# Kernel optimization log

Hardware: AMD Instinct MI355X
Metric: run time of the kernel (lower is better)

Reference implementation:

```python
import jax, jax.numpy as jnp
import numpy as np

G = 4       # num_groups
EPS = 1e-5  # BatchNorm eps


def setup_inputs() -> dict:
    key = jax.random.key(0)
    ks = jax.random.split(key, 8)
    B, C, T, V, K = 64, 256, 128, 25, 3
    dk = C // (G * 4)  # reduce_ratio=4 -> dk=16, dk*G=64
    return {
        "x": jax.random.normal(ks[0], (B, C, T, V), dtype=jnp.float32),
        "A": jax.random.uniform(ks[1], (K, V, V), dtype=jnp.float32),
        "Wq": jax.random.normal(ks[2], (dk * G, C), dtype=jnp.float32) * 0.05,
        "Wk": jax.random.normal(ks[3], (dk * G, C), dtype=jnp.float32) * 0.05,
        "Wconv": jax.random.normal(ks[4], (K, G, C // G, C // G), dtype=jnp.float32) * 0.05,
        "alpha": jnp.full((1,), 0.1, dtype=jnp.float32),
        "gamma": jax.random.uniform(ks[5], (C,), dtype=jnp.float32) + 0.5,
        "beta": jax.random.normal(ks[6], (C,), dtype=jnp.float32) * 0.1,
        "running_mean": jnp.zeros((C,), dtype=jnp.float32),
        "running_var": jnp.ones((C,), dtype=jnp.float32),
    }


def reference(x, A, Wq, Wk, Wconv, alpha, gamma, beta, running_mean, running_var):
    B, C, T, V = x.shape
    K = A.shape[0]
    dk = Wq.shape[0] // G
    Cg = C // G

    # Row-normalized fixed adjacency subsets (done in torch __init__)
    A_norm = A / jnp.clip(A.sum(-1, keepdims=True), 1e-6)  # (K,V,V)

    # Q/K 1x1 convs, temporal mean, per-group attention over joints
    q = jnp.einsum('oc,bctv->bov', Wq, x) / T  # conv then mean over T
    k = jnp.einsum('oc,bctv->bov', Wk, x) / T
    q = q.reshape(B, G, dk, V)
    k = k.reshape(B, G, dk, V)
    A_dyn = jnp.einsum('bgdv,bgdw->bgvw', q, k) / jnp.sqrt(jnp.float32(dk))
    A_dyn = jax.nn.softmax(A_dyn, axis=-1).mean(axis=1)  # (B,V,V)

    al = jnp.tanh(alpha[0])
    out = jnp.zeros_like(x)
    for k_idx in range(K):
        A_k = A_norm[k_idx][None] + al * A_dyn               # (B,V,V)
        x_agg = jnp.einsum('bvw,bctw->bctv', A_k, x)         # spatial aggregation
        xg = x_agg.reshape(B, G, Cg, T, V)
        y = jnp.einsum('goc,bgctv->bgotv', Wconv[k_idx], xg).reshape(B, C, T, V)
        out = out + y

    # BatchNorm2d in eval mode (running stats)
    inv = gamma / jnp.sqrt(running_var + EPS)
    bn = out * inv[None, :, None, None] + (beta - running_mean * inv)[None, :, None, None]
    return x + bn
```

## Files before the change

kernel.cpp:

```cpp
#include <hip/hip_runtime.h>

typedef __bf16 bf16x8 __attribute__((ext_vector_type(8)));
typedef __bf16 bf16x4 __attribute__((ext_vector_type(4)));
typedef float  f32x4  __attribute__((ext_vector_type(4)));


__global__ __launch_bounds__(256)
void k_tmean4(const float* __restrict__ x, float* __restrict__ xm)
{
    const int bid = blockIdx.x;
    const int b = bid >> 7, c2 = bid & 127;
    const int tid = threadIdx.x;
    const int c_loc = tid >> 7, r = tid & 127;

    __shared__ float xpart[2][25][5][4];

    if (r < 125) {
        const float* base = x + (size_t)(b * 256 + c2 * 2 + c_loc) * 3200;
        f32x4 acc = {0.f, 0.f, 0.f, 0.f};
#pragma unroll
        for (int i = 0; i < 7; ++i) {
            const int q = r + 125 * i;
            if (q < 800) {
                f32x4 v4 = *(const f32x4*)(base + q * 4);
                acc += v4;
            }
        }
        const int vq = r % 25, jg = r / 25;
        *(f32x4*)(&xpart[c_loc][vq][jg][0]) = acc;
    }
    __syncthreads();
    if (tid < 50) {
        const int cl = tid / 25, v = tid - cl * 25;
        float s = 0.f;
#pragma unroll
        for (int e = 0; e < 4; ++e) {
            const int vq = (((v - e + 25) % 25) * 19) % 25;
#pragma unroll
            for (int j = 0; j < 5; ++j) s += xpart[cl][vq][j][e];
        }
        xm[((size_t)(b * 256) + c2 * 2 + cl) * 25 + v] = s * (1.0f / 128.0f);
    }
}

__global__ __launch_bounds__(256)
void k_adyn(const float* __restrict__ xm, const float* __restrict__ A,
            const float* __restrict__ Wq, const float* __restrict__ Wk,
            const float* __restrict__ alpha, __bf16* __restrict__ afull,
            const float* __restrict__ Wconv, __bf16* __restrict__ wcb)
{
    const int b = blockIdx.x, tid = threadIdx.x;
    __shared__ float xm_s[256 * 25];
    __shared__ float q_s[64 * 25];
    __shared__ float k_s[64 * 25];
    __shared__ float sm_s[4][25][25];
    __shared__ float ad_s[25][25];
    __shared__ float rs_s[3][25];

    for (int i = tid; i < 768; i += 256)
        wcb[b * 768 + i] = (__bf16)Wconv[b * 768 + i];

    for (int i = tid; i < 256 * 25; i += 256) xm_s[i] = xm[(size_t)b * 6400 + i];
    for (int i = tid; i < 75; i += 256) {
        int k3 = i / 25, v = i - (i / 25) * 25;
        float s = 0.f;
        for (int w = 0; w < 25; ++w) s += A[(k3 * 25 + v) * 25 + w];
        rs_s[k3][v] = fmaxf(s, 1e-6f);
    }
    __syncthreads();

    for (int i = tid; i < 1600; i += 256) {
        int o = i / 25, v = i - o * 25;
        const float* wq = Wq + o * 256;
        const float* wk = Wk + o * 256;
        float aq = 0.f, ak = 0.f;
        for (int c4 = 0; c4 < 256; c4 += 4) {
            f32x4 q4 = *(const f32x4*)(wq + c4);
            f32x4 k4 = *(const f32x4*)(wk + c4);
#pragma unroll
            for (int e = 0; e < 4; ++e) {
                const float xv = xm_s[(c4 + e) * 25 + v];
                aq += q4[e] * xv;
                ak += k4[e] * xv;
            }
        }
        q_s[i] = aq; k_s[i] = ak;
    }
    __syncthreads();

    if (tid < 100) {
        int g = tid / 25, v = tid - (tid / 25) * 25;
        float l[25];
#pragma unroll
        for (int w = 0; w < 25; ++w) {
            float s = 0.f;
#pragma unroll
            for (int d = 0; d < 16; ++d)
                s += q_s[(g * 16 + d) * 25 + v] * k_s[(g * 16 + d) * 25 + w];
            l[w] = s * 0.25f;
        }
        float mx = l[0];
#pragma unroll
        for (int w = 1; w < 25; ++w) mx = fmaxf(mx, l[w]);
        float den = 0.f;
#pragma unroll
        for (int w = 0; w < 25; ++w) { l[w] = expf(l[w] - mx); den += l[w]; }
        float rden = 1.f / den;
#pragma unroll
        for (int w = 0; w < 25; ++w) sm_s[g][v][w] = l[w] * rden;
    }
    __syncthreads();
    for (int i = tid; i < 625; i += 256) {
        int v = i / 25, w = i - (i / 25) * 25;
        ad_s[v][w] = 0.25f * (sm_s[0][v][w] + sm_s[1][v][w] + sm_s[2][v][w] + sm_s[3][v][w]);
    }
    __syncthreads();

    const float al = tanhf(alpha[0]);
    for (int i = tid; i < 3 * 32 * 32; i += 256) {
        int k3 = i >> 10, rem = i & 1023, v = rem >> 5, w = rem & 31;
        float val = 0.f;
        if (v < 25 && w < 25)
            val = A[(k3 * 25 + v) * 25 + w] / rs_s[k3][v] + al * ad_s[v][w];
        afull[(size_t)b * 3072 + i] = (__bf16)val;
    }
}

__global__ __launch_bounds__(256, 4)
void k_main7(const float* __restrict__ x, const __bf16* __restrict__ wcb,
             const __bf16* __restrict__ afull,
             const float* __restrict__ gamma, const float* __restrict__ beta,
             const float* __restrict__ rmean, const float* __restrict__ rvar,
             float* __restrict__ out)
{
    const int orig = ((blockIdx.x & 7) << 10) | (blockIdx.x >> 3);
    const int tt = orig & 31;
    const int g  = (orig >> 5) & 3;
    const int b  = orig >> 7;
    const int tid = threadIdx.x;
    const int wave = tid >> 6;
    const int lane = tid & 63;
    const int l15 = lane & 15;
    const int lg  = lane >> 4;

    __shared__ __bf16 xs[64 * 4 * 32];
    __shared__ __bf16 xagg[112 * 64];

    {
        const int c = tid >> 2, t = tid & 3;
        const float* p = x + ((size_t)(b * 256 + g * 64 + c) * 128 + tt * 4 + t) * 25;
        float r[25];
#pragma unroll
        for (int j = 0; j < 25; ++j) r[j] = p[j];
        const int rowg = (c * 4 + t) << 2;
        const int sw = c & 7;
#pragma unroll
        for (int ch = 0; ch < 4; ++ch) {
            bf16x8 h;
#pragma unroll
            for (int e = 0; e < 8; ++e) {
                const int v = ch * 8 + e;
                h[e] = (v < 25) ? (__bf16)r[v] : (__bf16)0.f;
            }
            *(bf16x8*)((char*)xs + (((rowg | ch) ^ sw) << 4)) = h;
        }
    }

    const int o_lane = (wave << 4) + l15;
    const int ch = g * 64 + o_lane;
    const float inv  = gamma[ch] / sqrtf(rvar[ch] + 1e-5f);
    const float bias = beta[ch] - rmean[ch] * inv;

    const __bf16* ab = afull + ((size_t)(b * 3) << 10) + l15 * 32 + lg * 8;
    const __bf16* wb = wcb + (size_t)(g * 64 + o_lane) * 64 + lg * 8;

    __syncthreads();

    bf16x8 xfrag[4];
#pragma unroll
    for (int m = 0; m < 4; ++m) {
        const int c = m * 16 + l15;
        xfrag[m] = *(const bf16x8*)((char*)xs +
                      (((((c * 4 + wave) << 2) | lg) ^ (c & 7)) << 4));
    }

    f32x4 acc[7];
#pragma unroll
    for (int i = 0; i < 7; ++i) acc[i] = (f32x4){0.f, 0.f, 0.f, 0.f};
    const f32x4 zero4 = {0.f, 0.f, 0.f, 0.f};

#pragma unroll
    for (int k3 = 0; k3 < 3; ++k3) {
        bf16x8 bA[2], wf[2];
        bA[0] = *(const bf16x8*)(ab + (size_t)k3 * 1024);
        bA[1] = *(const bf16x8*)(ab + (size_t)k3 * 1024 + 512);
        wf[0] = *(const bf16x8*)(wb + (size_t)k3 * 16384);
        wf[1] = *(const bf16x8*)(wb + (size_t)k3 * 16384 + 32);

        if (k3 > 0) __syncthreads();

#pragma unroll
        for (int m = 0; m < 4; ++m) {
#pragma unroll
            for (int n = 0; n < 2; ++n) {
                f32x4 d = __builtin_amdgcn_mfma_f32_16x16x32_bf16(xfrag[m], bA[n],
                                                                  zero4, 0, 0, 0);
                const int v = n * 16 + l15;
                if (v < 25) {
                    const int cc  = wave * 25 + v;
                    const int col = (m * 16 + lg * 4) ^ ((cc & 7) << 3);
                    bf16x4 h;
                    h[0] = (__bf16)d[0]; h[1] = (__bf16)d[1];
                    h[2] = (__bf16)d[2]; h[3] = (__bf16)d[3];
                    *(bf16x4*)((char*)xagg + cc * 128 + col * 2) = h;
                }
            }
        }
        __syncthreads();

#pragma unroll
        for (int mcc = 0; mcc < 7; ++mcc) {
            const int cc = mcc * 16 + l15;
            const int sw2 = (cc & 7) << 3;
#pragma unroll
            for (int ks = 0; ks < 2; ++ks) {
                const int col = (ks * 32 + lg * 8) ^ sw2;
                bf16x8 aF = *(const bf16x8*)((char*)xagg + cc * 128 + col * 2);
                acc[mcc] = __builtin_amdgcn_mfma_f32_16x16x32_bf16(aF, wf[ks],
                                                                   acc[mcc], 0, 0, 0);
            }
        }
        if (k3 < 2) __syncthreads();
    }

    const size_t obase = (size_t)(b * 256 + ch) * 3200 + tt * 100;
#pragma unroll
    for (int mcc = 0; mcc < 7; ++mcc) {
        const int cc0 = mcc * 16 + lg * 4;
        if (cc0 < 100) {
            f32x4 o4;
#pragma unroll
            for (int j = 0; j < 4; ++j) {
                const int cc = cc0 + j;
                const int t = cc / 25, v = cc - t * 25;
                const int gr = (((o_lane * 4 + t) << 2) | (v >> 3)) ^ (o_lane & 7);
                const float xr = (float)*(const __bf16*)((char*)xs + (gr << 4) + ((v & 7) << 1));
                o4[j] = xr + acc[mcc][j] * inv + bias;
            }
            *(f32x4*)(out + obase + cc0) = o4;
        }
    }
}

extern "C" void kernel_launch(void* const* d_in, const int* in_sizes, int n_in,
                              void* d_out, int out_size, void* d_ws, size_t ws_size,
                              hipStream_t stream) {
    const float* x     = (const float*)d_in[0];
    const float* A     = (const float*)d_in[1];
    const float* Wq    = (const float*)d_in[2];
    const float* Wk    = (const float*)d_in[3];
    const float* Wconv = (const float*)d_in[4];
    const float* alpha = (const float*)d_in[5];
    const float* gamma = (const float*)d_in[6];
    const float* beta  = (const float*)d_in[7];
    const float* rmean = (const float*)d_in[8];
    const float* rvar  = (const float*)d_in[9];
    float* out = (float*)d_out;

    float*  xm    = (float*)d_ws;
    __bf16* afull = (__bf16*)((char*)d_ws + 1638400);
    __bf16* wcb   = (__bf16*)((char*)d_ws + 2031616);

    k_tmean4<<<64 * 128, 256, 0, stream>>>(x, xm);
    k_adyn<<<64, 256, 0, stream>>>(xm, A, Wq, Wk, alpha, afull, Wconv, wcb);
    k_main7<<<64 * 4 * 32, 256, 0, stream>>>(x, wcb, afull, gamma, beta,
                                             rmean, rvar, out);
}
```

Measured before the change: 193.0 us.

## Process two time tiles per block with prefetch of the next x tile

Each block of the main kernel now handles two consecutive 4-step time tiles instead of one, halving the grid size. The global load of the second tile's x values into registers is issued during the first tile's compute and then written to shared memory after the first output store. The aim is to hide global load latency and amortize per-block setup (BN params, weight/adjacency fragments) across two tiles. The cost is more register pressure from the extra 25-float prefetch buffer, extra barriers, and fewer blocks to fill the GPU.

New measurement: 344.8 us. 1.79x slower.

```diff
diff --git a/kernel.cpp b/kernel.cpp
--- a/kernel.cpp
+++ b/kernel.cpp
@@ -127,16 +127,16 @@
 }
 
 __global__ __launch_bounds__(256, 4)
-void k_main7(const float* __restrict__ x, const __bf16* __restrict__ wcb,
-             const __bf16* __restrict__ afull,
-             const float* __restrict__ gamma, const float* __restrict__ beta,
-             const float* __restrict__ rmean, const float* __restrict__ rvar,
-             float* __restrict__ out)
+void k_main11(const float* __restrict__ x, const __bf16* __restrict__ wcb,
+              const __bf16* __restrict__ afull,
+              const float* __restrict__ gamma, const float* __restrict__ beta,
+              const float* __restrict__ rmean, const float* __restrict__ rvar,
+              float* __restrict__ out)
 {
-    const int orig = ((blockIdx.x & 7) << 10) | (blockIdx.x >> 3);
-    const int tt = orig & 31;
-    const int g  = (orig >> 5) & 3;
-    const int b  = orig >> 7;
+    const int orig = ((blockIdx.x & 7) << 9) | (blockIdx.x >> 3);
+    const int tt2 = orig & 15;
+    const int g   = (orig >> 4) & 3;
+    const int b   = orig >> 6;
     const int tid = threadIdx.x;
     const int wave = tid >> 6;
     const int lane = tid & 63;
@@ -146,14 +146,14 @@
     __shared__ __bf16 xs[64 * 4 * 32];
     __shared__ __bf16 xagg[112 * 64];
 
+    const int c_st = tid >> 2, t_st = tid & 3;
+    const float* pbase = x + ((size_t)(b * 256 + g * 64 + c_st) * 128 + tt2 * 8 + t_st) * 25;
+    const int rowg = (c_st * 4 + t_st) << 2;
+    const int sw = c_st & 7;
     {
-        const int c = tid >> 2, t = tid & 3;
-        const float* p = x + ((size_t)(b * 256 + g * 64 + c) * 128 + tt * 4 + t) * 25;
         float r[25];
 #pragma unroll
-        for (int j = 0; j < 25; ++j) r[j] = p[j];
-        const int rowg = (c * 4 + t) << 2;
-        const int sw = c & 7;
+        for (int j = 0; j < 25; ++j) r[j] = pbase[j];
 #pragma unroll
         for (int ch = 0; ch < 4; ++ch) {
             bf16x8 h;
@@ -167,87 +167,112 @@
     }
 
     const int o_lane = (wave << 4) + l15;
-    const int ch = g * 64 + o_lane;
-    const float inv  = gamma[ch] / sqrtf(rvar[ch] + 1e-5f);
-    const float bias = beta[ch] - rmean[ch] * inv;
+    const int ch_o = g * 64 + o_lane;
+    const float inv  = gamma[ch_o] / sqrtf(rvar[ch_o] + 1e-5f);
+    const float bias = beta[ch_o] - rmean[ch_o] * inv;
 
     const __bf16* ab = afull + ((size_t)(b * 3) << 10) + l15 * 32 + lg * 8;
     const __bf16* wb = wcb + (size_t)(g * 64 + o_lane) * 64 + lg * 8;
 
     __syncthreads();
 
-    bf16x8 xfrag[4];
-#pragma unroll
-    for (int m = 0; m < 4; ++m) {
-        const int c = m * 16 + l15;
-        xfrag[m] = *(const bf16x8*)((char*)xs +
-                      (((((c * 4 + wave) << 2) | lg) ^ (c & 7)) << 4));
-    }
-
-    f32x4 acc[7];
-#pragma unroll
-    for (int i = 0; i < 7; ++i) acc[i] = (f32x4){0.f, 0.f, 0.f, 0.f};
-    const f32x4 zero4 = {0.f, 0.f, 0.f, 0.f};
-
-#pragma unroll
-    for (int k3 = 0; k3 < 3; ++k3) {
-        bf16x8 bA[2], wf[2];
-        bA[0] = *(const bf16x8*)(ab + (size_t)k3 * 1024);
-        bA[1] = *(const bf16x8*)(ab + (size_t)k3 * 1024 + 512);
-        wf[0] = *(const bf16x8*)(wb + (size_t)k3 * 16384);
-        wf[1] = *(const bf16x8*)(wb + (size_t)k3 * 16384 + 32);
-
-        if (k3 > 0) __syncthreads();
-
+    float r2[25];
+
+#pragma unroll 1
+    for (int it = 0; it < 2; ++it) {
+        bf16x8 xfrag[4];
 #pragma unroll
         for (int m = 0; m < 4; ++m) {
-#pragma unroll
-            for (int n = 0; n < 2; ++n) {
-                f32x4 d = __builtin_amdgcn_mfma_f32_16x16x32_bf16(xfrag[m], bA[n],
-                                                                  zero4, 0, 0, 0);
-                const int v = n * 16 + l15;
-                if (v < 25) {
-                    const int cc  = wave * 25 + v;
-                    const int col = (m * 16 + lg * 4) ^ ((cc & 7) << 3);
-                    bf16x4 h;
-                    h[0] = (__bf16)d[0]; h[1] = (__bf16)d[1];
-                    h[2] = (__bf16)d[2]; h[3] = (__bf16)d[3];
-                    *(bf16x4*)((char*)xagg + cc * 128 + col * 2) = h;
+            const int c = m * 16 + l15;
+            xfrag[m] = *(const bf16x8*)((char*)xs +
+                          (((((c * 4 + wave) << 2) | lg) ^ (c & 7)) << 4));
+        }
+
+        if (it == 0) {
+#pragma unroll
+            for (int j = 0; j < 25; ++j) r2[j] = pbase[100 + j];
+        }
+
+        f32x4 acc[7];
+#pragma unroll
+        for (int i = 0; i < 7; ++i) acc[i] = (f32x4){0.f, 0.f, 0.f, 0.f};
+        const f32x4 zero4 = {0.f, 0.f, 0.f, 0.f};
+
+#pragma unroll
+        for (int k3 = 0; k3 < 3; ++k3) {
+            bf16x8 bA[2], wf[2];
+            bA[0] = *(const bf16x8*)(ab + (size_t)k3 * 1024);
+            bA[1] = *(const bf16x8*)(ab + (size_t)k3 * 1024 + 512);
+            wf[0] = *(const bf16x8*)(wb + (size_t)k3 * 16384);
+            wf[1] = *(const bf16x8*)(wb + (size_t)k3 * 16384 + 32);
+
+            if (k3 > 0) __syncthreads();
+
+#pragma unroll
+            for (int m = 0; m < 4; ++m) {
+#pragma unroll
+                for (int n = 0; n < 2; ++n) {
+                    f32x4 d = __builtin_amdgcn_mfma_f32_16x16x32_bf16(xfrag[m], bA[n],
+                                                                      zero4, 0, 0, 0);
+                    const int v = n * 16 + l15;
+                    if (v < 25) {
+                        const int cc  = wave * 25 + v;
+                        const int col = (m * 16 + lg * 4) ^ ((cc & 7) << 3);
+                        bf16x4 h;
+                        h[0] = (__bf16)d[0]; h[1] = (__bf16)d[1];
+                        h[2] = (__bf16)d[2]; h[3] = (__bf16)d[3];
+                        *(bf16x4*)((char*)xagg + cc * 128 + col * 2) = h;
+                    }
                 }
             }
-        }
-        __syncthreads();
-
+            __syncthreads();
+
+#pragma unroll
+            for (int mcc = 0; mcc < 7; ++mcc) {
+                const int cc = mcc * 16 + l15;
+                const int sw2 = (cc & 7) << 3;
+#pragma unroll
+                for (int ks = 0; ks < 2; ++ks) {
+                    const int col = (ks * 32 + lg * 8) ^ sw2;
+                    bf16x8 aF = *(const bf16x8*)((char*)xagg + cc * 128 + col * 2);
+                    acc[mcc] = __builtin_amdgcn_mfma_f32_16x16x32_bf16(aF, wf[ks],
+                                                                       acc[mcc], 0, 0, 0);
+                }
+            }
+            if (k3 < 2) __syncthreads();
+        }
+
+        const size_t obase = (size_t)(b * 256 + ch_o) * 3200 + (tt2 * 2 + it) * 100;
 #pragma unroll
         for (int mcc = 0; mcc < 7; ++mcc) {
-            const int cc = mcc * 16 + l15;
-            const int sw2 = (cc & 7) << 3;
-#pragma unroll
-            for (int ks = 0; ks < 2; ++ks) {
-                const int col = (ks * 32 + lg * 8) ^ sw2;
-                bf16x8 aF = *(const bf16x8*)((char*)xagg + cc * 128 + col * 2);
-                acc[mcc] = __builtin_amdgcn_mfma_f32_16x16x32_bf16(aF, wf[ks],
-                                                                   acc[mcc], 0, 0, 0);
-            }
-        }
-        if (k3 < 2) __syncthreads();
-    }
-
-    const size_t obase = (size_t)(b * 256 + ch) * 3200 + tt * 100;
-#pragma unroll
-    for (int mcc = 0; mcc < 7; ++mcc) {
-        const int cc0 = mcc * 16 + lg * 4;
-        if (cc0 < 100) {
-            f32x4 o4;
-#pragma unroll
-            for (int j = 0; j < 4; ++j) {
-                const int cc = cc0 + j;
-                const int t = cc / 25, v = cc - t * 25;
-                const int gr = (((o_lane * 4 + t) << 2) | (v >> 3)) ^ (o_lane & 7);
-                const float xr = (float)*(const __bf16*)((char*)xs + (gr << 4) + ((v & 7) << 1));
-                o4[j] = xr + acc[mcc][j] * inv + bias;
-            }
-            *(f32x4*)(out + obase + cc0) = o4;
+            const int cc0 = mcc * 16 + lg * 4;
+            if (cc0 < 100) {
+                f32x4 o4;
+#pragma unroll
+                for (int j = 0; j < 4; ++j) {
+                    const int cc = cc0 + j;
+                    const int t = cc / 25, v = cc - t * 25;
+                    const int gr = (((o_lane * 4 + t) << 2) | (v >> 3)) ^ (o_lane & 7);
+                    const float xr = (float)*(const __bf16*)((char*)xs + (gr << 4) + ((v & 7) << 1));
+                    o4[j] = xr + acc[mcc][j] * inv + bias;
+                }
+                *(f32x4*)(out + obase + cc0) = o4;
+            }
+        }
+
+        if (it == 0) {
+            __syncthreads();
+#pragma unroll
+            for (int chq = 0; chq < 4; ++chq) {
+                bf16x8 h;
+#pragma unroll
+                for (int e = 0; e < 8; ++e) {
+                    const int v = chq * 8 + e;
+                    h[e] = (v < 25) ? (__bf16)r2[v] : (__bf16)0.f;
+                }
+                *(bf16x8*)((char*)xs + (((rowg | chq) ^ sw) << 4)) = h;
+            }
+            __syncthreads();
         }
     }
 }
@@ -273,6 +298,6 @@
 
     k_tmean4<<<64 * 128, 256, 0, stream>>>(x, xm);
     k_adyn<<<64, 256, 0, stream>>>(xm, A, Wq, Wk, alpha, afull, Wconv, wcb);
-    k_main7<<<64 * 4 * 32, 256, 0, stream>>>(x, wcb, afull, gamma, beta,
-                                             rmean, rvar, out);
+    k_main11<<<64 * 4 * 16, 256, 0, stream>>>(x, wcb, afull, gamma, beta,
+                                              rmean, rvar, out);
 }
```
